# Kernel optimization log

Hardware: AMD Instinct MI355X
Metric: run time of the kernel (lower is better)

Reference implementation:

```python
import jax, jax.numpy as jnp
import numpy as np

KSIZE = 7
LOSS_WEIGHT = 1.0


def _box_filter(x, ksize):
    # x: (N, 1, H, W) already reflect-padded -> valid conv with ones kernel
    kern = jnp.ones((1, 1, ksize, ksize), x.dtype)
    return jax.lax.conv_general_dilated(
        x, kern, window_strides=(1, 1), padding='VALID',
        dimension_numbers=('NCHW', 'OIHW', 'NCHW'))


def _local_var(residual, ksize):
    # unbiased variance over each ksize x ksize window (reflect padding),
    # computed via box-filtered sum and sum-of-squares (same math as
    # torch.var over unfolded windows, without materializing the windows).
    pad = (ksize - 1) // 2
    rp = jnp.pad(residual, ((0, 0), (0, 0), (pad, pad), (pad, pad)), mode='reflect')
    n = ksize * ksize
    s = _box_filter(rp, ksize)        # window sums
    ss = _box_filter(rp * rp, ksize)  # window sums of squares
    return (ss - s * s / n) / (n - 1)


def setup_inputs() -> dict:
    key = jax.random.key(0)
    k1, k2 = jax.random.split(key)
    shape = (16, 3, 512, 512)
    pred = jax.random.normal(k1, shape, dtype=jnp.float32)
    target = jax.random.normal(k2, shape, dtype=jnp.float32)
    return {"pred": pred, "target": target}


def reference(pred, target):
    # residual over channels: (N, 1, H, W)
    residual = jnp.sum(jnp.abs(target - pred), axis=1, keepdims=True)
    # patch-level weight: unbiased var over (C,H,W), ^(1/5)
    patch_w = jnp.var(residual, axis=(1, 2, 3), keepdims=True, ddof=1) ** 0.2
    # pixel-level weight: local unbiased variance in ksize window
    pixel_w = _local_var(residual, KSIZE)
    overall_weight = patch_w * pixel_w  # (N, 1, H, W), broadcasts over C
    # L1 criterion on weighted pred vs weighted target
    return jnp.mean(jnp.abs(overall_weight * pred - overall_weight * target)) * LOSS_WEIGHT
```

## Files before the change

kernel.cpp:

```cpp
#include <hip/hip_runtime.h>
#include <math.h>

#define N_IMG 16
#define C_CH 3
#define H_DIM 512
#define W_DIM 512
#define HW (H_DIM * W_DIM)
#define KS 7
#define PAD 3

#define TSX 64
#define TSY 32
#define TILE_H (TSY + 2 * PAD)
#define TSTRIDE 72
#define TPB 256
#define TILES_X (W_DIM / TSX)
#define TILES_Y (H_DIM / TSY)
#define TILES_PER_IMG (TILES_X * TILES_Y)
#define NBLOCKS (N_IMG * TILES_PER_IMG)

__device__ __forceinline__ int reflect_i(int g, int n) {
    return (g < 0) ? -g : ((g >= n) ? (2 * n - 2 - g) : g);
}

__global__ __launch_bounds__(TPB) void k_fused(const float* __restrict__ pred,
                                               const float* __restrict__ targ,
                                               float* __restrict__ pr,
                                               float* __restrict__ pr2,
                                               float* __restrict__ pc) {
    __shared__ __align__(16) float tile[TILE_H * TSTRIDE];

    const int bid = blockIdx.x;
    const int n   = bid >> 7;
    const int t   = bid & 127;
    const int by  = t >> 3;
    const int bx  = t & 7;
    const int tid = threadIdx.x;

    const int y0 = by * TSY - PAD;

    const float*  pb = pred + (size_t)n * C_CH * HW;
    const float*  qb = targ + (size_t)n * C_CH * HW;
    const float4* P  = (const float4*)pb;
    const float4* Q  = (const float4*)qb;
    const int PL4 = HW / 4;

#pragma unroll
    for (int it = 0; it < 3; ++it) {
        const int s = tid + it * TPB;
        if (it < 2 || tid < 96) {
            const int row = s >> 4;
            const int c4  = s & 15;
            const int gy  = reflect_i(y0 + row, H_DIM);
            const int off = gy * (W_DIM / 4) + bx * 16 + c4;
            const float4 p0 = P[off], p1 = P[off + PL4], p2 = P[off + 2 * PL4];
            const float4 q0 = Q[off], q1 = Q[off + PL4], q2 = Q[off + 2 * PL4];
            float4 r;
            r.x = fabsf(q0.x - p0.x) + fabsf(q1.x - p1.x) + fabsf(q2.x - p2.x);
            r.y = fabsf(q0.y - p0.y) + fabsf(q1.y - p1.y) + fabsf(q2.y - p2.y);
            r.z = fabsf(q0.z - p0.z) + fabsf(q1.z - p1.z) + fabsf(q2.z - p2.z);
            r.w = fabsf(q0.w - p0.w) + fabsf(q1.w - p1.w) + fabsf(q2.w - p2.w);
            *(float4*)&tile[row * TSTRIDE + 4 + c4 * 4] = r;
        }
    }
    if (tid < TILE_H * 6) {
        const int row = tid / 6;
        const int k   = tid - row * 6;
        const int lx  = (k < 3) ? (1 + k) : (65 + k);
        const int gx  = reflect_i(bx * TSX + lx - 4, W_DIM);
        const int gy  = reflect_i(y0 + row, H_DIM);
        const int off = gy * W_DIM + gx;
        tile[row * TSTRIDE + lx] = fabsf(qb[off] - pb[off])
                                 + fabsf(qb[off + HW] - pb[off + HW])
                                 + fabsf(qb[off + 2 * HW] - pb[off + 2 * HW]);
    }
    __syncthreads();

    const int tx = tid & 63;
    const int r0 = (tid >> 6) << 3;

    float rS[KS], rSS[KS];
    float S = 0.f, SS = 0.f;
#pragma unroll
    for (int d = 0; d < KS; ++d) {
        const float* rw = &tile[(r0 + d) * TSTRIDE + 1 + tx];
        float s = 0.f, ss = 0.f;
#pragma unroll
        for (int j = 0; j < KS; ++j) { const float v = rw[j]; s += v; ss += v * v; }
        rS[d] = s; rSS[d] = ss; S += s; SS += ss;
    }

    float acc_r = 0.f, acc_r2 = 0.f, acc_c = 0.f;
#pragma unroll
    for (int k = 0; k < 8; ++k) {
        if (k > 0) {
            const float* rw = &tile[(r0 + 6 + k) * TSTRIDE + 1 + tx];
            float s = 0.f, ss = 0.f;
#pragma unroll
            for (int j = 0; j < KS; ++j) { const float v = rw[j]; s += v; ss += v * v; }
            S  += s  - rS[k - 1];
            SS += ss - rSS[k - 1];
        }
        const float pix_var = (SS - S * S * (1.0f / 49.0f)) * (1.0f / 48.0f);
        const float center  = tile[(r0 + k + 3) * TSTRIDE + 4 + tx];
        acc_r  += center;
        acc_r2 += center * center;
        acc_c  += pix_var * center;
    }

#pragma unroll
    for (int off = 32; off > 0; off >>= 1) {
        acc_r  += __shfl_down(acc_r,  off);
        acc_r2 += __shfl_down(acc_r2, off);
        acc_c  += __shfl_down(acc_c,  off);
    }
    __shared__ float sh_r[4], sh_r2[4], sh_c[4];
    const int lane = tid & 63;
    const int wave = tid >> 6;
    if (lane == 0) { sh_r[wave] = acc_r; sh_r2[wave] = acc_r2; sh_c[wave] = acc_c; }
    __syncthreads();
    if (tid == 0) {
        pr [bid] = sh_r [0] + sh_r [1] + sh_r [2] + sh_r [3];
        pr2[bid] = sh_r2[0] + sh_r2[1] + sh_r2[2] + sh_r2[3];
        pc [bid] = sh_c [0] + sh_c [1] + sh_c [2] + sh_c [3];
    }
}

__global__ void k_final(const float* __restrict__ pr,
                        const float* __restrict__ pr2,
                        const float* __restrict__ pc,
                        float* __restrict__ out) {
    __shared__ double sh[N_IMG];
    const int tid  = threadIdx.x;
    const int w    = tid >> 6;
    const int lane = tid & 63;

    double R = 0.0, R2 = 0.0, Cs = 0.0;
    for (int i = lane; i < TILES_PER_IMG; i += 64) {
        const int idx = w * TILES_PER_IMG + i;
        R  += (double)pr[idx];
        R2 += (double)pr2[idx];
        Cs += (double)pc[idx];
    }
#pragma unroll
    for (int off = 32; off > 0; off >>= 1) {
        R  += __shfl_down(R,  off);
        R2 += __shfl_down(R2, off);
        Cs += __shfl_down(Cs, off);
    }
    if (lane == 0) {
        const double pvar = (R2 - R * R / (double)HW) / (double)(HW - 1);
        sh[w] = pow(pvar, 0.2) * Cs;
    }
    __syncthreads();
    if (tid == 0) {
        double s = 0.0;
        for (int i = 0; i < N_IMG; ++i) s += sh[i];
        out[0] = (float)(s / ((double)N_IMG * C_CH * HW));
    }
}

extern "C" void kernel_launch(void* const* d_in, const int* in_sizes, int n_in,
                              void* d_out, int out_size, void* d_ws, size_t ws_size,
                              hipStream_t stream) {
    const float* pred = (const float*)d_in[0];
    const float* targ = (const float*)d_in[1];

    float* pr  = (float*)d_ws;
    float* pr2 = pr  + NBLOCKS;
    float* pc  = pr2 + NBLOCKS;
    float* out = (float*)d_out;

    k_fused<<<NBLOCKS, TPB, 0, stream>>>(pred, targ, pr, pr2, pc);
    k_final<<<1, 1024, 0, stream>>>(pr, pr2, pc, out);
}
```

Baseline: 127.4 us.

## Batch global loads before compute and fold final reduction into last block

All pred/target loads for the tile and its halo are issued into registers before any residual arithmetic, to raise memory-level parallelism. The separate finalize kernel is removed: each block bumps an atomic counter after writing its partials, and the last block performs the per-image variance and final mean. This removes a kernel launch but adds a memset, an atomic and threadfences, and raises register pressure.

Measured after the change: 225.3 us. 1.77x slower.

```diff
diff --git a/kernel.cpp b/kernel.cpp
--- a/kernel.cpp
+++ b/kernel.cpp
@@ -14,9 +14,7 @@
 #define TILE_H (TSY + 2 * PAD)
 #define TSTRIDE 72
 #define TPB 256
-#define TILES_X (W_DIM / TSX)
-#define TILES_Y (H_DIM / TSY)
-#define TILES_PER_IMG (TILES_X * TILES_Y)
+#define TILES_PER_IMG 128
 #define NBLOCKS (N_IMG * TILES_PER_IMG)
 
 __device__ __forceinline__ int reflect_i(int g, int n) {
@@ -27,7 +25,9 @@
                                                const float* __restrict__ targ,
                                                float* __restrict__ pr,
                                                float* __restrict__ pr2,
-                                               float* __restrict__ pc) {
+                                               float* __restrict__ pc,
+                                               unsigned int* __restrict__ counter,
+                                               float* __restrict__ out) {
     __shared__ __align__(16) float tile[TILE_H * TSTRIDE];
 
     const int bid = blockIdx.x;
@@ -36,8 +36,7 @@
     const int by  = t >> 3;
     const int bx  = t & 7;
     const int tid = threadIdx.x;
-
-    const int y0 = by * TSY - PAD;
+    const int y0  = by * TSY - PAD;
 
     const float*  pb = pred + (size_t)n * C_CH * HW;
     const float*  qb = targ + (size_t)n * C_CH * HW;
@@ -45,35 +44,49 @@
     const float4* Q  = (const float4*)qb;
     const int PL4 = HW / 4;
 
+    float4 pv[3][3], qv[3][3];
+    int irow[3], ic4[3];
+    const bool act2 = (tid < 96);
 #pragma unroll
     for (int it = 0; it < 3; ++it) {
-        const int s = tid + it * TPB;
-        if (it < 2 || tid < 96) {
-            const int row = s >> 4;
-            const int c4  = s & 15;
+        const int s   = tid + it * TPB;
+        const int row = s >> 4;
+        const int c4  = s & 15;
+        irow[it] = row; ic4[it] = c4;
+        if (it < 2 || act2) {
             const int gy  = reflect_i(y0 + row, H_DIM);
             const int off = gy * (W_DIM / 4) + bx * 16 + c4;
-            const float4 p0 = P[off], p1 = P[off + PL4], p2 = P[off + 2 * PL4];
-            const float4 q0 = Q[off], q1 = Q[off + PL4], q2 = Q[off + 2 * PL4];
-            float4 r;
-            r.x = fabsf(q0.x - p0.x) + fabsf(q1.x - p1.x) + fabsf(q2.x - p2.x);
-            r.y = fabsf(q0.y - p0.y) + fabsf(q1.y - p1.y) + fabsf(q2.y - p2.y);
-            r.z = fabsf(q0.z - p0.z) + fabsf(q1.z - p1.z) + fabsf(q2.z - p2.z);
-            r.w = fabsf(q0.w - p0.w) + fabsf(q1.w - p1.w) + fabsf(q2.w - p2.w);
-            *(float4*)&tile[row * TSTRIDE + 4 + c4 * 4] = r;
+            pv[it][0] = P[off]; pv[it][1] = P[off + PL4]; pv[it][2] = P[off + 2 * PL4];
+            qv[it][0] = Q[off]; qv[it][1] = Q[off + PL4]; qv[it][2] = Q[off + 2 * PL4];
         }
     }
-    if (tid < TILE_H * 6) {
-        const int row = tid / 6;
-        const int k   = tid - row * 6;
-        const int lx  = (k < 3) ? (1 + k) : (65 + k);
-        const int gx  = reflect_i(bx * TSX + lx - 4, W_DIM);
-        const int gy  = reflect_i(y0 + row, H_DIM);
+    const bool hact = (tid < TILE_H * 6);
+    float hp0 = 0.f, hp1 = 0.f, hp2 = 0.f, hq0 = 0.f, hq1 = 0.f, hq2 = 0.f;
+    int hrow = 0, hlx = 0;
+    if (hact) {
+        hrow = tid / 6;
+        const int k = tid - hrow * 6;
+        hlx = (k < 3) ? (1 + k) : (65 + k);
+        const int gx  = reflect_i(bx * TSX + hlx - 4, W_DIM);
+        const int gy  = reflect_i(y0 + hrow, H_DIM);
         const int off = gy * W_DIM + gx;
-        tile[row * TSTRIDE + lx] = fabsf(qb[off] - pb[off])
-                                 + fabsf(qb[off + HW] - pb[off + HW])
-                                 + fabsf(qb[off + 2 * HW] - pb[off + 2 * HW]);
+        hp0 = pb[off]; hp1 = pb[off + HW]; hp2 = pb[off + 2 * HW];
+        hq0 = qb[off]; hq1 = qb[off + HW]; hq2 = qb[off + 2 * HW];
     }
+
+#pragma unroll
+    for (int it = 0; it < 3; ++it) {
+        if (it < 2 || act2) {
+            float4 r;
+            r.x = fabsf(qv[it][0].x - pv[it][0].x) + fabsf(qv[it][1].x - pv[it][1].x) + fabsf(qv[it][2].x - pv[it][2].x);
+            r.y = fabsf(qv[it][0].y - pv[it][0].y) + fabsf(qv[it][1].y - pv[it][1].y) + fabsf(qv[it][2].y - pv[it][2].y);
+            r.z = fabsf(qv[it][0].z - pv[it][0].z) + fabsf(qv[it][1].z - pv[it][1].z) + fabsf(qv[it][2].z - pv[it][2].z);
+            r.w = fabsf(qv[it][0].w - pv[it][0].w) + fabsf(qv[it][1].w - pv[it][1].w) + fabsf(qv[it][2].w - pv[it][2].w);
+            *(float4*)&tile[irow[it] * TSTRIDE + 4 + ic4[it] * 4] = r;
+        }
+    }
+    if (hact)
+        tile[hrow * TSTRIDE + hlx] = fabsf(hq0 - hp0) + fabsf(hq1 - hp1) + fabsf(hq2 - hp2);
     __syncthreads();
 
     const int tx = tid & 63;
@@ -115,6 +128,7 @@
         acc_c  += __shfl_down(acc_c,  off);
     }
     __shared__ float sh_r[4], sh_r2[4], sh_c[4];
+    __shared__ int lastflag;
     const int lane = tid & 63;
     const int wave = tid >> 6;
     if (lane == 0) { sh_r[wave] = acc_r; sh_r2[wave] = acc_r2; sh_c[wave] = acc_c; }
@@ -123,40 +137,42 @@
         pr [bid] = sh_r [0] + sh_r [1] + sh_r [2] + sh_r [3];
         pr2[bid] = sh_r2[0] + sh_r2[1] + sh_r2[2] + sh_r2[3];
         pc [bid] = sh_c [0] + sh_c [1] + sh_c [2] + sh_c [3];
-    }
-}
-
-__global__ void k_final(const float* __restrict__ pr,
-                        const float* __restrict__ pr2,
-                        const float* __restrict__ pc,
-                        float* __restrict__ out) {
-    __shared__ double sh[N_IMG];
-    const int tid  = threadIdx.x;
-    const int w    = tid >> 6;
-    const int lane = tid & 63;
-
-    double R = 0.0, R2 = 0.0, Cs = 0.0;
-    for (int i = lane; i < TILES_PER_IMG; i += 64) {
-        const int idx = w * TILES_PER_IMG + i;
-        R  += (double)pr[idx];
-        R2 += (double)pr2[idx];
-        Cs += (double)pc[idx];
-    }
-#pragma unroll
-    for (int off = 32; off > 0; off >>= 1) {
-        R  += __shfl_down(R,  off);
-        R2 += __shfl_down(R2, off);
-        Cs += __shfl_down(Cs, off);
-    }
-    if (lane == 0) {
-        const double pvar = (R2 - R * R / (double)HW) / (double)(HW - 1);
-        sh[w] = pow(pvar, 0.2) * Cs;
+        __threadfence();
+        const unsigned prev = atomicAdd(counter, 1u);
+        lastflag = (prev == NBLOCKS - 1);
     }
     __syncthreads();
-    if (tid == 0) {
-        double s = 0.0;
-        for (int i = 0; i < N_IMG; ++i) s += sh[i];
-        out[0] = (float)(s / ((double)N_IMG * C_CH * HW));
+
+    if (lastflag) {
+        __threadfence();
+        double local = 0.0;
+#pragma unroll
+        for (int im4 = 0; im4 < 4; ++im4) {
+            const int im = wave * 4 + im4;
+            double R = 0.0, R2 = 0.0, Cs = 0.0;
+            for (int i = lane; i < TILES_PER_IMG; i += 64) {
+                const int idx = im * TILES_PER_IMG + i;
+                R  += (double)pr[idx];
+                R2 += (double)pr2[idx];
+                Cs += (double)pc[idx];
+            }
+#pragma unroll
+            for (int off = 32; off > 0; off >>= 1) {
+                R  += __shfl_down(R,  off);
+                R2 += __shfl_down(R2, off);
+                Cs += __shfl_down(Cs, off);
+            }
+            if (lane == 0) {
+                const double pvar = (R2 - R * R / (double)HW) / (double)(HW - 1);
+                local += pow(pvar, 0.2) * Cs;
+            }
+        }
+        __shared__ double shd[4];
+        if (lane == 0) shd[wave] = local;
+        __syncthreads();
+        if (tid == 0)
+            out[0] = (float)((shd[0] + shd[1] + shd[2] + shd[3])
+                             / ((double)N_IMG * C_CH * HW));
     }
 }
 
@@ -166,11 +182,12 @@
     const float* pred = (const float*)d_in[0];
     const float* targ = (const float*)d_in[1];
 
-    float* pr  = (float*)d_ws;
-    float* pr2 = pr  + NBLOCKS;
-    float* pc  = pr2 + NBLOCKS;
-    float* out = (float*)d_out;
+    float*    pr      = (float*)d_ws;
+    float*    pr2     = pr  + NBLOCKS;
+    float*    pc      = pr2 + NBLOCKS;
+    unsigned* counter = (unsigned*)(pc + NBLOCKS);
+    float*    out     = (float*)d_out;
 
-    k_fused<<<NBLOCKS, TPB, 0, stream>>>(pred, targ, pr, pr2, pc);
-    k_final<<<1, 1024, 0, stream>>>(pr, pr2, pc, out);
+    hipMemsetAsync(counter, 0, sizeof(unsigned), stream);
+    k_fused<<<NBLOCKS, TPB, 0, stream>>>(pred, targ, pr, pr2, pc, counter, out);
 }
```

## Split fused kernel into residual pass and local-variance pass via workspace buffer

Applied to the files above, without the earlier changes.

The single fused kernel is split in two. The first kernel computes the channel-summed residual, writes it to a global workspace and produces per-block sum and sum-of-squares partials. The second kernel reads the residual with its halo to compute the local-variance weighted sum. The aim is to stop re-reading the six input planes for the halo rows (38/32 overlap) and to simplify the stencil kernel, at the cost of an extra 16 MB write and read of the residual plus one more kernel launch.

After: 130.2 us. +2.1%, slower.

```diff
diff --git a/kernel.cpp b/kernel.cpp
--- a/kernel.cpp
+++ b/kernel.cpp
@@ -6,28 +6,85 @@
 #define H_DIM 512
 #define W_DIM 512
 #define HW (H_DIM * W_DIM)
+#define HW4 (HW / 4)
 #define KS 7
 #define PAD 3
+
+#define ABLOCKS 2048
+#define A_PER_IMG (ABLOCKS / N_IMG)
 
 #define TSX 64
 #define TSY 32
 #define TILE_H (TSY + 2 * PAD)
 #define TSTRIDE 72
 #define TPB 256
-#define TILES_X (W_DIM / TSX)
-#define TILES_Y (H_DIM / TSY)
-#define TILES_PER_IMG (TILES_X * TILES_Y)
-#define NBLOCKS (N_IMG * TILES_PER_IMG)
+#define TILES_PER_IMG 128
+#define BBLOCKS (N_IMG * TILES_PER_IMG)
 
 __device__ __forceinline__ int reflect_i(int g, int n) {
     return (g < 0) ? -g : ((g >= n) ? (2 * n - 2 - g) : g);
 }
 
-__global__ __launch_bounds__(TPB) void k_fused(const float* __restrict__ pred,
-                                               const float* __restrict__ targ,
+__global__ __launch_bounds__(TPB) void k_resid(const float4* __restrict__ pred,
+                                               const float4* __restrict__ targ,
+                                               float4* __restrict__ resid,
                                                float* __restrict__ pr,
-                                               float* __restrict__ pr2,
-                                               float* __restrict__ pc) {
+                                               float* __restrict__ pr2) {
+    const int bid = blockIdx.x;
+    const int tid = threadIdx.x;
+    const int n   = bid >> 7;
+    const int o0  = (bid & 127) * 512 + tid;
+    const int b4  = n * C_CH * HW4;
+
+    const float4 pa0 = pred[b4 + o0];
+    const float4 pb0 = pred[b4 + HW4 + o0];
+    const float4 pc0 = pred[b4 + 2 * HW4 + o0];
+    const float4 qa0 = targ[b4 + o0];
+    const float4 qb0 = targ[b4 + HW4 + o0];
+    const float4 qc0 = targ[b4 + 2 * HW4 + o0];
+    const int o1 = o0 + 256;
+    const float4 pa1 = pred[b4 + o1];
+    const float4 pb1 = pred[b4 + HW4 + o1];
+    const float4 pc1 = pred[b4 + 2 * HW4 + o1];
+    const float4 qa1 = targ[b4 + o1];
+    const float4 qb1 = targ[b4 + HW4 + o1];
+    const float4 qc1 = targ[b4 + 2 * HW4 + o1];
+
+    float4 r0, r1;
+    r0.x = fabsf(qa0.x - pa0.x) + fabsf(qb0.x - pb0.x) + fabsf(qc0.x - pc0.x);
+    r0.y = fabsf(qa0.y - pa0.y) + fabsf(qb0.y - pb0.y) + fabsf(qc0.y - pc0.y);
+    r0.z = fabsf(qa0.z - pa0.z) + fabsf(qb0.z - pb0.z) + fabsf(qc0.z - pc0.z);
+    r0.w = fabsf(qa0.w - pa0.w) + fabsf(qb0.w - pb0.w) + fabsf(qc0.w - pc0.w);
+    r1.x = fabsf(qa1.x - pa1.x) + fabsf(qb1.x - pb1.x) + fabsf(qc1.x - pc1.x);
+    r1.y = fabsf(qa1.y - pa1.y) + fabsf(qb1.y - pb1.y) + fabsf(qc1.y - pc1.y);
+    r1.z = fabsf(qa1.z - pa1.z) + fabsf(qb1.z - pb1.z) + fabsf(qc1.z - pc1.z);
+    r1.w = fabsf(qa1.w - pa1.w) + fabsf(qb1.w - pb1.w) + fabsf(qc1.w - pc1.w);
+
+    resid[n * HW4 + o0] = r0;
+    resid[n * HW4 + o1] = r1;
+
+    float s  = r0.x + r0.y + r0.z + r0.w + r1.x + r1.y + r1.z + r1.w;
+    float ss = r0.x * r0.x + r0.y * r0.y + r0.z * r0.z + r0.w * r0.w
+             + r1.x * r1.x + r1.y * r1.y + r1.z * r1.z + r1.w * r1.w;
+
+#pragma unroll
+    for (int off = 32; off > 0; off >>= 1) {
+        s  += __shfl_down(s,  off);
+        ss += __shfl_down(ss, off);
+    }
+    __shared__ float sh_s[4], sh_ss[4];
+    const int lane = tid & 63;
+    const int wave = tid >> 6;
+    if (lane == 0) { sh_s[wave] = s; sh_ss[wave] = ss; }
+    __syncthreads();
+    if (tid == 0) {
+        pr [bid] = sh_s [0] + sh_s [1] + sh_s [2] + sh_s [3];
+        pr2[bid] = sh_ss[0] + sh_ss[1] + sh_ss[2] + sh_ss[3];
+    }
+}
+
+__global__ __launch_bounds__(TPB) void k_lvar(const float* __restrict__ resid,
+                                              float* __restrict__ pc) {
     __shared__ __align__(16) float tile[TILE_H * TSTRIDE];
 
     const int bid = blockIdx.x;
@@ -36,14 +93,10 @@
     const int by  = t >> 3;
     const int bx  = t & 7;
     const int tid = threadIdx.x;
-
-    const int y0 = by * TSY - PAD;
-
-    const float*  pb = pred + (size_t)n * C_CH * HW;
-    const float*  qb = targ + (size_t)n * C_CH * HW;
-    const float4* P  = (const float4*)pb;
-    const float4* Q  = (const float4*)qb;
-    const int PL4 = HW / 4;
+    const int y0  = by * TSY - PAD;
+
+    const float*  rb = resid + (size_t)n * HW;
+    const float4* R4 = (const float4*)rb;
 
 #pragma unroll
     for (int it = 0; it < 3; ++it) {
@@ -52,15 +105,8 @@
             const int row = s >> 4;
             const int c4  = s & 15;
             const int gy  = reflect_i(y0 + row, H_DIM);
-            const int off = gy * (W_DIM / 4) + bx * 16 + c4;
-            const float4 p0 = P[off], p1 = P[off + PL4], p2 = P[off + 2 * PL4];
-            const float4 q0 = Q[off], q1 = Q[off + PL4], q2 = Q[off + 2 * PL4];
-            float4 r;
-            r.x = fabsf(q0.x - p0.x) + fabsf(q1.x - p1.x) + fabsf(q2.x - p2.x);
-            r.y = fabsf(q0.y - p0.y) + fabsf(q1.y - p1.y) + fabsf(q2.y - p2.y);
-            r.z = fabsf(q0.z - p0.z) + fabsf(q1.z - p1.z) + fabsf(q2.z - p2.z);
-            r.w = fabsf(q0.w - p0.w) + fabsf(q1.w - p1.w) + fabsf(q2.w - p2.w);
-            *(float4*)&tile[row * TSTRIDE + 4 + c4 * 4] = r;
+            const float4 v = R4[gy * (W_DIM / 4) + bx * 16 + c4];
+            *(float4*)&tile[row * TSTRIDE + 4 + c4 * 4] = v;
         }
     }
     if (tid < TILE_H * 6) {
@@ -69,10 +115,7 @@
         const int lx  = (k < 3) ? (1 + k) : (65 + k);
         const int gx  = reflect_i(bx * TSX + lx - 4, W_DIM);
         const int gy  = reflect_i(y0 + row, H_DIM);
-        const int off = gy * W_DIM + gx;
-        tile[row * TSTRIDE + lx] = fabsf(qb[off] - pb[off])
-                                 + fabsf(qb[off + HW] - pb[off + HW])
-                                 + fabsf(qb[off + 2 * HW] - pb[off + 2 * HW]);
+        tile[row * TSTRIDE + lx] = rb[gy * W_DIM + gx];
     }
     __syncthreads();
 
@@ -90,7 +133,7 @@
         rS[d] = s; rSS[d] = ss; S += s; SS += ss;
     }
 
-    float acc_r = 0.f, acc_r2 = 0.f, acc_c = 0.f;
+    float acc_c = 0.f;
 #pragma unroll
     for (int k = 0; k < 8; ++k) {
         if (k > 0) {
@@ -103,27 +146,20 @@
         }
         const float pix_var = (SS - S * S * (1.0f / 49.0f)) * (1.0f / 48.0f);
         const float center  = tile[(r0 + k + 3) * TSTRIDE + 4 + tx];
-        acc_r  += center;
-        acc_r2 += center * center;
-        acc_c  += pix_var * center;
-    }
-
-#pragma unroll
-    for (int off = 32; off > 0; off >>= 1) {
-        acc_r  += __shfl_down(acc_r,  off);
-        acc_r2 += __shfl_down(acc_r2, off);
-        acc_c  += __shfl_down(acc_c,  off);
-    }
-    __shared__ float sh_r[4], sh_r2[4], sh_c[4];
+        acc_c += pix_var * center;
+    }
+
+#pragma unroll
+    for (int off = 32; off > 0; off >>= 1)
+        acc_c += __shfl_down(acc_c, off);
+
+    __shared__ float sh_c[4];
     const int lane = tid & 63;
     const int wave = tid >> 6;
-    if (lane == 0) { sh_r[wave] = acc_r; sh_r2[wave] = acc_r2; sh_c[wave] = acc_c; }
-    __syncthreads();
-    if (tid == 0) {
-        pr [bid] = sh_r [0] + sh_r [1] + sh_r [2] + sh_r [3];
-        pr2[bid] = sh_r2[0] + sh_r2[1] + sh_r2[2] + sh_r2[3];
-        pc [bid] = sh_c [0] + sh_c [1] + sh_c [2] + sh_c [3];
-    }
+    if (lane == 0) sh_c[wave] = acc_c;
+    __syncthreads();
+    if (tid == 0)
+        pc[bid] = sh_c[0] + sh_c[1] + sh_c[2] + sh_c[3];
 }
 
 __global__ void k_final(const float* __restrict__ pr,
@@ -136,12 +172,13 @@
     const int lane = tid & 63;
 
     double R = 0.0, R2 = 0.0, Cs = 0.0;
-    for (int i = lane; i < TILES_PER_IMG; i += 64) {
-        const int idx = w * TILES_PER_IMG + i;
-        R  += (double)pr[idx];
-        R2 += (double)pr2[idx];
-        Cs += (double)pc[idx];
-    }
+    for (int i = lane; i < A_PER_IMG; i += 64) {
+        R  += (double)pr [w * A_PER_IMG + i];
+        R2 += (double)pr2[w * A_PER_IMG + i];
+    }
+    for (int i = lane; i < TILES_PER_IMG; i += 64)
+        Cs += (double)pc[w * TILES_PER_IMG + i];
+
 #pragma unroll
     for (int off = 32; off > 0; off >>= 1) {
         R  += __shfl_down(R,  off);
@@ -163,14 +200,16 @@
 extern "C" void kernel_launch(void* const* d_in, const int* in_sizes, int n_in,
                               void* d_out, int out_size, void* d_ws, size_t ws_size,
                               hipStream_t stream) {
-    const float* pred = (const float*)d_in[0];
-    const float* targ = (const float*)d_in[1];
-
-    float* pr  = (float*)d_ws;
-    float* pr2 = pr  + NBLOCKS;
-    float* pc  = pr2 + NBLOCKS;
-    float* out = (float*)d_out;
-
-    k_fused<<<NBLOCKS, TPB, 0, stream>>>(pred, targ, pr, pr2, pc);
+    const float4* pred = (const float4*)d_in[0];
+    const float4* targ = (const float4*)d_in[1];
+
+    float4* resid = (float4*)d_ws;
+    float*  pr    = (float*)((char*)d_ws + (size_t)N_IMG * HW * sizeof(float));
+    float*  pr2   = pr  + ABLOCKS;
+    float*  pc    = pr2 + ABLOCKS;
+    float*  out   = (float*)d_out;
+
+    k_resid<<<ABLOCKS, TPB, 0, stream>>>(pred, targ, resid, pr, pr2);
+    k_lvar <<<BBLOCKS, TPB, 0, stream>>>((const float*)resid, pc);
     k_final<<<1, 1024, 0, stream>>>(pr, pr2, pc, out);
 }
```

## Process two tiles per block with register prefetch and double-buffered LDS

Applied to the files above, without the earlier changes.

Each block now handles two adjacent tiles, halving the grid. The global loads for the second tile are issued into registers before the stencil on the first tile runs, and LDS is double-buffered, so load latency can overlap compute. The cost is higher register pressure from holding 18 float4 values per thread, which may lower occupancy. The final reduction is also changed to expect 64 partials per image.

Result: no change. 127.5 us (+0.1%).

```diff
diff --git a/kernel.cpp b/kernel.cpp
--- a/kernel.cpp
+++ b/kernel.cpp
@@ -6,6 +6,7 @@
 #define H_DIM 512
 #define W_DIM 512
 #define HW (H_DIM * W_DIM)
+#define HW4 (HW / 4)
 #define KS 7
 #define PAD 3
 
@@ -14,36 +15,33 @@
 #define TILE_H (TSY + 2 * PAD)
 #define TSTRIDE 72
 #define TPB 256
-#define TILES_X (W_DIM / TSX)
-#define TILES_Y (H_DIM / TSY)
-#define TILES_PER_IMG (TILES_X * TILES_Y)
-#define NBLOCKS (N_IMG * TILES_PER_IMG)
+#define TPT 2
+#define TILES_PER_IMG 128
+#define NTILES (N_IMG * TILES_PER_IMG)
+#define NBLOCKS (NTILES / TPT)
+#define BLK_PER_IMG (NBLOCKS / N_IMG)
 
 __device__ __forceinline__ int reflect_i(int g, int n) {
     return (g < 0) ? -g : ((g >= n) ? (2 * n - 2 - g) : g);
 }
 
-__global__ __launch_bounds__(TPB) void k_fused(const float* __restrict__ pred,
-                                               const float* __restrict__ targ,
-                                               float* __restrict__ pr,
-                                               float* __restrict__ pr2,
-                                               float* __restrict__ pc) {
-    __shared__ __align__(16) float tile[TILE_H * TSTRIDE];
-
-    const int bid = blockIdx.x;
-    const int n   = bid >> 7;
-    const int t   = bid & 127;
-    const int by  = t >> 3;
-    const int bx  = t & 7;
-    const int tid = threadIdx.x;
-
+struct TileRegs {
+    float4 pv[3][3], qv[3][3];
+    float  hp[3], hq[3];
+};
+
+__device__ __forceinline__ void load_tile(int tile, int tid,
+                                          const float4* __restrict__ pred4,
+                                          const float4* __restrict__ targ4,
+                                          const float* __restrict__ predf,
+                                          const float* __restrict__ targf,
+                                          TileRegs& R) {
+    const int n  = tile >> 7;
+    const int t  = tile & 127;
+    const int by = t >> 3;
+    const int bx = t & 7;
     const int y0 = by * TSY - PAD;
-
-    const float*  pb = pred + (size_t)n * C_CH * HW;
-    const float*  qb = targ + (size_t)n * C_CH * HW;
-    const float4* P  = (const float4*)pb;
-    const float4* Q  = (const float4*)qb;
-    const int PL4 = HW / 4;
+    const int b4 = n * C_CH * HW4;
 
 #pragma unroll
     for (int it = 0; it < 3; ++it) {
@@ -52,15 +50,13 @@
             const int row = s >> 4;
             const int c4  = s & 15;
             const int gy  = reflect_i(y0 + row, H_DIM);
-            const int off = gy * (W_DIM / 4) + bx * 16 + c4;
-            const float4 p0 = P[off], p1 = P[off + PL4], p2 = P[off + 2 * PL4];
-            const float4 q0 = Q[off], q1 = Q[off + PL4], q2 = Q[off + 2 * PL4];
-            float4 r;
-            r.x = fabsf(q0.x - p0.x) + fabsf(q1.x - p1.x) + fabsf(q2.x - p2.x);
-            r.y = fabsf(q0.y - p0.y) + fabsf(q1.y - p1.y) + fabsf(q2.y - p2.y);
-            r.z = fabsf(q0.z - p0.z) + fabsf(q1.z - p1.z) + fabsf(q2.z - p2.z);
-            r.w = fabsf(q0.w - p0.w) + fabsf(q1.w - p1.w) + fabsf(q2.w - p2.w);
-            *(float4*)&tile[row * TSTRIDE + 4 + c4 * 4] = r;
+            const int off = b4 + gy * (W_DIM / 4) + bx * 16 + c4;
+            R.pv[it][0] = pred4[off];
+            R.pv[it][1] = pred4[off + HW4];
+            R.pv[it][2] = pred4[off + 2 * HW4];
+            R.qv[it][0] = targ4[off];
+            R.qv[it][1] = targ4[off + HW4];
+            R.qv[it][2] = targ4[off + 2 * HW4];
         }
     }
     if (tid < TILE_H * 6) {
@@ -69,13 +65,40 @@
         const int lx  = (k < 3) ? (1 + k) : (65 + k);
         const int gx  = reflect_i(bx * TSX + lx - 4, W_DIM);
         const int gy  = reflect_i(y0 + row, H_DIM);
-        const int off = gy * W_DIM + gx;
-        tile[row * TSTRIDE + lx] = fabsf(qb[off] - pb[off])
-                                 + fabsf(qb[off + HW] - pb[off + HW])
-                                 + fabsf(qb[off + 2 * HW] - pb[off + 2 * HW]);
-    }
-    __syncthreads();
-
+        const int off = n * C_CH * HW + gy * W_DIM + gx;
+#pragma unroll
+        for (int c = 0; c < 3; ++c) { R.hp[c] = predf[off + c * HW]; R.hq[c] = targf[off + c * HW]; }
+    }
+}
+
+__device__ __forceinline__ void store_tile(float* __restrict__ buf, int tid,
+                                           const TileRegs& R) {
+#pragma unroll
+    for (int it = 0; it < 3; ++it) {
+        const int s = tid + it * TPB;
+        if (it < 2 || tid < 96) {
+            const int row = s >> 4;
+            const int c4  = s & 15;
+            float4 r;
+            r.x = fabsf(R.qv[it][0].x - R.pv[it][0].x) + fabsf(R.qv[it][1].x - R.pv[it][1].x) + fabsf(R.qv[it][2].x - R.pv[it][2].x);
+            r.y = fabsf(R.qv[it][0].y - R.pv[it][0].y) + fabsf(R.qv[it][1].y - R.pv[it][1].y) + fabsf(R.qv[it][2].y - R.pv[it][2].y);
+            r.z = fabsf(R.qv[it][0].z - R.pv[it][0].z) + fabsf(R.qv[it][1].z - R.pv[it][1].z) + fabsf(R.qv[it][2].z - R.pv[it][2].z);
+            r.w = fabsf(R.qv[it][0].w - R.pv[it][0].w) + fabsf(R.qv[it][1].w - R.pv[it][1].w) + fabsf(R.qv[it][2].w - R.pv[it][2].w);
+            *(float4*)&buf[row * TSTRIDE + 4 + c4 * 4] = r;
+        }
+    }
+    if (tid < TILE_H * 6) {
+        const int row = tid / 6;
+        const int k   = tid - row * 6;
+        const int lx  = (k < 3) ? (1 + k) : (65 + k);
+        buf[row * TSTRIDE + lx] = fabsf(R.hq[0] - R.hp[0])
+                                + fabsf(R.hq[1] - R.hp[1])
+                                + fabsf(R.hq[2] - R.hp[2]);
+    }
+}
+
+__device__ __forceinline__ void stencil(const float* __restrict__ buf, int tid,
+                                        float& acc_r, float& acc_r2, float& acc_c) {
     const int tx = tid & 63;
     const int r0 = (tid >> 6) << 3;
 
@@ -83,18 +106,16 @@
     float S = 0.f, SS = 0.f;
 #pragma unroll
     for (int d = 0; d < KS; ++d) {
-        const float* rw = &tile[(r0 + d) * TSTRIDE + 1 + tx];
+        const float* rw = &buf[(r0 + d) * TSTRIDE + 1 + tx];
         float s = 0.f, ss = 0.f;
 #pragma unroll
         for (int j = 0; j < KS; ++j) { const float v = rw[j]; s += v; ss += v * v; }
         rS[d] = s; rSS[d] = ss; S += s; SS += ss;
     }
-
-    float acc_r = 0.f, acc_r2 = 0.f, acc_c = 0.f;
 #pragma unroll
     for (int k = 0; k < 8; ++k) {
         if (k > 0) {
-            const float* rw = &tile[(r0 + 6 + k) * TSTRIDE + 1 + tx];
+            const float* rw = &buf[(r0 + 6 + k) * TSTRIDE + 1 + tx];
             float s = 0.f, ss = 0.f;
 #pragma unroll
             for (int j = 0; j < KS; ++j) { const float v = rw[j]; s += v; ss += v * v; }
@@ -102,10 +123,37 @@
             SS += ss - rSS[k - 1];
         }
         const float pix_var = (SS - S * S * (1.0f / 49.0f)) * (1.0f / 48.0f);
-        const float center  = tile[(r0 + k + 3) * TSTRIDE + 4 + tx];
+        const float center  = buf[(r0 + k + 3) * TSTRIDE + 4 + tx];
         acc_r  += center;
         acc_r2 += center * center;
         acc_c  += pix_var * center;
+    }
+}
+
+__global__ __launch_bounds__(TPB) void k_fused(const float4* __restrict__ pred4,
+                                               const float4* __restrict__ targ4,
+                                               const float* __restrict__ predf,
+                                               const float* __restrict__ targf,
+                                               float* __restrict__ pr,
+                                               float* __restrict__ pr2,
+                                               float* __restrict__ pc) {
+    __shared__ __align__(16) float buf[2][TILE_H * TSTRIDE];
+
+    const int bid = blockIdx.x;
+    const int tid = threadIdx.x;
+    const int tb0 = bid * TPT;
+
+    TileRegs R;
+    load_tile(tb0, tid, pred4, targ4, predf, targf, R);
+
+    float acc_r = 0.f, acc_r2 = 0.f, acc_c = 0.f;
+#pragma unroll
+    for (int t = 0; t < TPT; ++t) {
+        store_tile(buf[t & 1], tid, R);
+        __syncthreads();
+        if (t + 1 < TPT)
+            load_tile(tb0 + t + 1, tid, pred4, targ4, predf, targf, R);
+        stencil(buf[t & 1], tid, acc_r, acc_r2, acc_c);
     }
 
 #pragma unroll
@@ -136,11 +184,11 @@
     const int lane = tid & 63;
 
     double R = 0.0, R2 = 0.0, Cs = 0.0;
-    for (int i = lane; i < TILES_PER_IMG; i += 64) {
-        const int idx = w * TILES_PER_IMG + i;
-        R  += (double)pr[idx];
-        R2 += (double)pr2[idx];
-        Cs += (double)pc[idx];
+    if (lane < BLK_PER_IMG) {
+        const int idx = w * BLK_PER_IMG + lane;
+        R  = (double)pr[idx];
+        R2 = (double)pr2[idx];
+        Cs = (double)pc[idx];
     }
 #pragma unroll
     for (int off = 32; off > 0; off >>= 1) {
@@ -163,14 +211,15 @@
 extern "C" void kernel_launch(void* const* d_in, const int* in_sizes, int n_in,
                               void* d_out, int out_size, void* d_ws, size_t ws_size,
                               hipStream_t stream) {
-    const float* pred = (const float*)d_in[0];
-    const float* targ = (const float*)d_in[1];
+    const float* predf = (const float*)d_in[0];
+    const float* targf = (const float*)d_in[1];
 
     float* pr  = (float*)d_ws;
     float* pr2 = pr  + NBLOCKS;
     float* pc  = pr2 + NBLOCKS;
     float* out = (float*)d_out;
 
-    k_fused<<<NBLOCKS, TPB, 0, stream>>>(pred, targ, pr, pr2, pc);
+    k_fused<<<NBLOCKS, TPB, 0, stream>>>((const float4*)predf, (const float4*)targf,
+                                         predf, targf, pr, pr2, pc);
     k_final<<<1, 1024, 0, stream>>>(pr, pr2, pc, out);
 }
```
